# Performance work log

Measured on AMD Instinct MI355X. Metric: run time of the kernel, lower is better.

The kernel has to match this reference:

```python
import jax, jax.numpy as jnp
import numpy as np

DET_SIZE = 5120
DET_THRESHOLD = 0.5
NMS_THRESHOLD = 0.4
STRIDES = (8, 16, 32)
NUM_ANCHORS = 2
TOP_K = 2048  # fixed pre-NMS candidate count (jit-friendly stand-in for torch.where filtering)


def _anchor_centers(stride):
    n = DET_SIZE // stride
    g = jnp.arange(n, dtype=jnp.float32) * stride
    X, Y = jnp.meshgrid(g, g, indexing='xy')       # matches torch.meshgrid(..., indexing='xy')
    c = jnp.stack([X, Y], axis=-1).reshape(-1, 2)  # (n*n, 2), x fastest
    return jnp.repeat(c, NUM_ANCHORS, axis=0)      # stack([c]*2, dim=1).reshape(-1,2) == interleaved repeat


def _pairwise_iou(b):
    # b: (K,4) xyxy
    area = jnp.clip(b[:, 2] - b[:, 0], 0.0) * jnp.clip(b[:, 3] - b[:, 1], 0.0)
    lt = jnp.maximum(b[:, None, :2], b[None, :, :2])
    rb = jnp.minimum(b[:, None, 2:], b[None, :, 2:])
    wh = jnp.clip(rb - lt, 0.0)
    inter = wh[..., 0] * wh[..., 1]
    return inter / (area[:, None] + area[None, :] - inter + 1e-9)


def _forward(scores8, bbox8, lms8, scores16, bbox16, lms16, scores32, bbox32, lms32, det_scale):
    confs, boxes, lmss = [], [], []
    per_stride = [(scores8, bbox8, lms8), (scores16, bbox16, lms16), (scores32, bbox32, lms32)]
    for (conf, bbox, lms), stride in zip(per_stride, STRIDES):
        c = _anchor_centers(stride)                 # (N,2)
        b = bbox * stride                            # distance-style offsets scaled by stride
        l = lms * stride
        box = jnp.concatenate([c - b[:, :2], c + b[:, 2:4]], axis=-1) / det_scale  # (N,4) xyxy
        pts = (c[:, None, :] + l.reshape(-1, 5, 2)) / det_scale                    # (N,5,2)
        confs.append(conf.reshape(-1)); boxes.append(box); lmss.append(pts)
    conf = jnp.concatenate(confs)
    box = jnp.concatenate(boxes, axis=0)
    pts = jnp.concatenate(lmss, axis=0)
    # score threshold via masking (fixed shapes); below-threshold entries get conf=-1
    conf_m = jnp.where(conf >= DET_THRESHOLD, conf, -1.0)
    top_conf, top_idx = jax.lax.top_k(conf_m, TOP_K)
    top_box = box[top_idx]          # (K,4)
    top_pts = pts[top_idx]          # (K,5,2)
    valid = top_conf >= DET_THRESHOLD
    iou = _pairwise_iou(top_box)    # (K,K)
    later = jnp.arange(TOP_K)
    def body(i, keep):
        supp = (iou[i] > NMS_THRESHOLD) & (later > i) & keep[i] & valid[i]
        return keep & ~supp
    keep = jax.lax.fori_loop(0, TOP_K, body, valid)  # greedy NMS in descending-score order
    m = keep.astype(top_box.dtype)
    # (K, 15) = [conf | bbox(4) | lms(10)], suppressed/invalid rows zeroed
    return jnp.concatenate([(top_conf * m)[:, None], top_box * m[:, None], top_pts.reshape(TOP_K, 10) * m[:, None]], axis=-1)


def setup_inputs() -> dict:
    key = jax.random.key(0)
    ks = jax.random.split(key, 9)
    inp = {}
    for i, s in enumerate(STRIDES):
        n = DET_SIZE // s
        N = n * n * NUM_ANCHORS
        inp[f'scores{s}'] = jax.random.uniform(ks[3 * i], (N,), dtype=jnp.float32)
        inp[f'bbox{s}'] = jax.random.uniform(ks[3 * i + 1], (N, 4), dtype=jnp.float32) * 8.0
        inp[f'lms{s}'] = jax.random.normal(ks[3 * i + 2], (N, 10), dtype=jnp.float32) * 4.0
    inp['det_scale'] = jnp.array(0.5, dtype=jnp.float32)
    return inp


def reference(scores8, bbox8, lms8, scores16, bbox16, lms16, scores32, bbox32, lms32, det_scale):
    return _forward(scores8, bbox8, lms8, scores16, bbox16, lms16, scores32, bbox32, lms32, det_scale)
```

## Files before the change

kernel.cpp:

```cpp
#include <hip/hip_runtime.h>
#include <stdint.h>
#include <stddef.h>

#pragma clang fp contract(off)

#define N8   819200u
#define N16  204800u
#define N32  51200u
#define NTOT 1075200u
#define TOPK 2048
#define CAND_MAX 8192
#define NBIN 8192u
#define BINSHIFT 10
#define NMS_THR 0.4f
#define DET_THR 0.5f

#define OFF_HIST   0u
#define OFF_META   32768u
#define OFF_CAND   32832u
#define OFF_TIDX   98368u
#define OFF_TCONF  106560u
#define OFF_BOX    114752u
#define OFF_DIAG   147520u
#define OFF_SUPPT  155968u

__device__ __forceinline__ float load_conf(unsigned a, const float* __restrict__ s8,
                                           const float* __restrict__ s16,
                                           const float* __restrict__ s32) {
  if (a < N8) return s8[a];
  if (a < N8 + N16) return s16[a - N8];
  return s32[a - (N8 + N16)];
}

__device__ __forceinline__ void decode(unsigned a,
    const float* __restrict__ b8, const float* __restrict__ l8,
    const float* __restrict__ b16, const float* __restrict__ l16,
    const float* __restrict__ b32, const float* __restrict__ l32,
    float& cx, float& cy, float& s, const float*& bb, const float*& lm) {
  if (a < N8) {
    unsigned cell = a >> 1;
    cx = (float)((cell % 640u) * 8u); cy = (float)((cell / 640u) * 8u);
    s = 8.f; bb = b8 + (size_t)a * 4; lm = l8 + (size_t)a * 10;
  } else if (a < N8 + N16) {
    unsigned loc = a - N8; unsigned cell = loc >> 1;
    cx = (float)((cell % 320u) * 16u); cy = (float)((cell / 320u) * 16u);
    s = 16.f; bb = b16 + (size_t)loc * 4; lm = l16 + (size_t)loc * 10;
  } else {
    unsigned loc = a - (N8 + N16); unsigned cell = loc >> 1;
    cx = (float)((cell % 160u) * 32u); cy = (float)((cell / 160u) * 32u);
    s = 32.f; bb = b32 + (size_t)loc * 4; lm = l32 + (size_t)loc * 10;
  }
}

__global__ void k_hist(const float* __restrict__ s8, const float* __restrict__ s16,
                       const float* __restrict__ s32, unsigned* __restrict__ hist) {
  unsigned i = blockIdx.x * blockDim.x + threadIdx.x;
  unsigned st = gridDim.x * blockDim.x;
  for (unsigned a = i; a < NTOT; a += st) {
    float c = load_conf(a, s8, s16, s32);
    if (c >= DET_THR) {
      unsigned v = (__float_as_uint(c) - 0x3F000000u) >> BINSHIFT;
      if (v > NBIN - 1u) v = NBIN - 1u;
      atomicAdd(&hist[v], 1u);
    }
  }
}

__global__ void __launch_bounds__(1024) k_scan(const unsigned* __restrict__ hist,
                                               unsigned* __restrict__ meta) {
  __shared__ unsigned suf[1024];
  int t = threadIdx.x;
  const unsigned* hp = hist + (size_t)t * 8;
  unsigned s = 0;
  for (int b = 0; b < 8; b++) s += hp[b];
  suf[t] = s;
  __syncthreads();
  for (int d = 1; d < 1024; d <<= 1) {
    unsigned v = (t + d < 1024) ? suf[t + d] : 0u;
    __syncthreads();
    suf[t] += v;
    __syncthreads();
  }
  unsigned total = suf[0];
  unsigned mine = suf[t];
  unsigned nxt = (t < 1023) ? suf[t + 1] : 0u;
  if (total < (unsigned)TOPK) {
    if (t == 0) { meta[0] = 0u; meta[2] = total; }
    return;
  }
  if (mine >= (unsigned)TOPK && nxt < (unsigned)TOPK) {
    unsigned run = nxt, cut = (unsigned)t * 8u;
    for (int b = 7; b >= 0; b--) {
      run += hp[b];
      if (run >= (unsigned)TOPK) { cut = (unsigned)t * 8u + (unsigned)b; break; }
    }
    meta[0] = cut; meta[2] = total;
  }
}

__global__ void k_compact(const float* __restrict__ s8, const float* __restrict__ s16,
                          const float* __restrict__ s32, unsigned* __restrict__ meta,
                          unsigned long long* __restrict__ cand) {
  unsigned cut = meta[0];
  unsigned i = blockIdx.x * blockDim.x + threadIdx.x;
  unsigned st = gridDim.x * blockDim.x;
  for (unsigned a = i; a < NTOT; a += st) {
    float c = load_conf(a, s8, s16, s32);
    if (c >= DET_THR) {
      unsigned b = __float_as_uint(c);
      unsigned v = (b - 0x3F000000u) >> BINSHIFT;
      if (v >= cut) {
        unsigned pos = atomicAdd(&meta[3], 1u);
        if (pos < (unsigned)CAND_MAX)
          cand[pos] = ((unsigned long long)b << 32) |
                      (unsigned long long)(0xFFFFFFFFu - a);
      }
    }
  }
}

__global__ void __launch_bounds__(256) k_rank(
    const unsigned long long* __restrict__ cand, const unsigned* __restrict__ meta,
    const float* __restrict__ b8, const float* __restrict__ l8,
    const float* __restrict__ b16, const float* __restrict__ l16,
    const float* __restrict__ b32, const float* __restrict__ l32,
    const float* __restrict__ dsp,
    unsigned* __restrict__ tidx, float* __restrict__ tconf, float* __restrict__ box) {
  unsigned count = meta[3];
  if (count > (unsigned)CAND_MAX) count = (unsigned)CAND_MAX;
  unsigned wave = blockIdx.x * 4u + (threadIdx.x >> 6);
  unsigned lane = threadIdx.x & 63u;
  if (wave >= count) return;
  unsigned long long my = cand[wave];
  unsigned cnt = 0;
  for (unsigned i = lane; i < count; i += 64u)
    cnt += (cand[i] > my) ? 1u : 0u;
  for (int d = 32; d > 0; d >>= 1) cnt += __shfl_down(cnt, d);
  if (lane == 0 && cnt < (unsigned)TOPK) {
    unsigned r = cnt;
    unsigned a = 0xFFFFFFFFu - (unsigned)(my & 0xFFFFFFFFull);
    float conf = __uint_as_float((unsigned)(my >> 32));
    float cx, cy, s; const float* bb; const float* lm;
    decode(a, b8, l8, b16, l16, b32, l32, cx, cy, s, bb, lm);
    float ds = dsp[0];
    float b0 = bb[0] * s, b1 = bb[1] * s, b2 = bb[2] * s, b3 = bb[3] * s;
    box[r * 4 + 0] = (cx - b0) / ds;
    box[r * 4 + 1] = (cy - b1) / ds;
    box[r * 4 + 2] = (cx + b2) / ds;
    box[r * 4 + 3] = (cy + b3) / ds;
    tidx[r] = a; tconf[r] = conf;
  }
}

__global__ void __launch_bounds__(256) k_supp(const float* __restrict__ box,
                                              unsigned* __restrict__ supp_t,
                                              unsigned* __restrict__ diag32) {
  int i = blockIdx.x;
  const float4 bi = ((const float4*)box)[i];
  float ai = fmaxf(bi.z - bi.x, 0.f) * fmaxf(bi.w - bi.y, 0.f);
  int tid = threadIdx.x;
  int lane = tid & 63, wv = tid >> 6;
  int c = i >> 5, k = i & 31;
  for (int base = 0; base < TOPK; base += 256) {
    int j = base + tid;
    const float4 bj = ((const float4*)box)[j];
    float aj = fmaxf(bj.z - bj.x, 0.f) * fmaxf(bj.w - bj.y, 0.f);
    float ltx = fmaxf(bi.x, bj.x), lty = fmaxf(bi.y, bj.y);
    float rbx = fminf(bi.z, bj.z), rby = fminf(bi.w, bj.w);
    float w = fmaxf(rbx - ltx, 0.f), h = fmaxf(rby - lty, 0.f);
    float inter = w * h;
    float iou = inter / (ai + aj - inter + 1e-9f);
    bool pred = (iou > NMS_THR) && (j > i);
    unsigned long long word = __ballot(pred);
    int w64 = (base >> 6) + wv;
    if (lane == 0) {
      supp_t[c * 2048 + (2 * w64) * 32 + k]     = (unsigned)(word & 0xFFFFFFFFull);
      supp_t[c * 2048 + (2 * w64 + 1) * 32 + k] = (unsigned)(word >> 32);
      if (w64 == (i >> 6))
        diag32[i] = (unsigned)(word >> (((i >> 5) & 1) * 32));
    }
  }
}

__global__ void __launch_bounds__(256) k_nms_out(
    const unsigned* __restrict__ supp_t, const unsigned* __restrict__ diag32,
    const unsigned* __restrict__ meta,
    const unsigned* __restrict__ tidx, const float* __restrict__ tconf,
    const float* __restrict__ b8, const float* __restrict__ l8,
    const float* __restrict__ b16, const float* __restrict__ l16,
    const float* __restrict__ b32, const float* __restrict__ l32,
    const float* __restrict__ dsp, float* __restrict__ out) {
  __shared__ unsigned keepw[64];
  int tid = threadIdx.x;
  if (tid < 64) {
    int lane = tid;
    unsigned count = meta[3];
    if (count > (unsigned)TOPK) count = (unsigned)TOPK;
    unsigned lo = (unsigned)lane * 32u;
    unsigned kw = (count >= lo + 32u) ? 0xFFFFFFFFu
                : (count <= lo ? 0u : ((1u << (count - lo)) - 1u));
    const uint4* rp4 = (const uint4*)supp_t + (size_t)lane * 8;
    uint4 T0[8], T1[8], T2[8], T3[8];
    unsigned dga[32], dgb[32];

#define LOADT(BUF, C)                                                         \
  _Pragma("unroll") for (int q = 0; q < 8; q++)                               \
      BUF[q] = rp4[(size_t)((C) * 512 + q)];
#define LOADD(DBUF, C)                                                        \
  _Pragma("unroll") for (int k = 0; k < 32; k++)                              \
      DBUF[k] = diag32[(unsigned)((C) * 32 + k)];

    LOADT(T0, 0) LOADT(T1, 1) LOADT(T2, 2) LOADT(T3, 3)
    LOADD(dga, 0)

#define STEP(BUF, DCUR, DNXT, C)                                              \
  {                                                                           \
    unsigned w = __builtin_amdgcn_readlane(kw, (C));                          \
    _Pragma("unroll") for (int k = 0; k < 32; k++) {                          \
      unsigned d = __builtin_amdgcn_readfirstlane(DCUR[k]);                   \
      w &= ~(((w >> k) & 1u) ? d : 0u);                                       \
    }                                                                         \
    if ((C) + 1 < 64) { LOADD(DNXT, (C) + 1) }                                \
    unsigned acc = 0u;                                                        \
    _Pragma("unroll") for (int q = 0; q < 8; q++) {                           \
      unsigned m0 = (unsigned)((int)(w << (31 - (4 * q + 0))) >> 31);         \
      unsigned m1 = (unsigned)((int)(w << (31 - (4 * q + 1))) >> 31);         \
      unsigned m2 = (unsigned)((int)(w << (31 - (4 * q + 2))) >> 31);         \
      unsigned m3 = (unsigned)((int)(w << (31 - (4 * q + 3))) >> 31);         \
      acc |= BUF[q].x & m0;                                                   \
      acc |= BUF[q].y & m1;                                                   \
      acc |= BUF[q].z & m2;                                                   \
      acc |= BUF[q].w & m3;                                                   \
    }                                                                         \
    kw &= ~acc;                                                               \
    if ((C) + 4 < 64) { LOADT(BUF, (C) + 4) }                                 \
  }

#pragma unroll 1
    for (int c = 0; c < 64; c += 8) {
      STEP(T0, dga, dgb, c + 0)
      STEP(T1, dgb, dga, c + 1)
      STEP(T2, dga, dgb, c + 2)
      STEP(T3, dgb, dga, c + 3)
      STEP(T0, dga, dgb, c + 4)
      STEP(T1, dgb, dga, c + 5)
      STEP(T2, dga, dgb, c + 6)
      STEP(T3, dgb, dga, c + 7)
    }
#undef LOADT
#undef LOADD
#undef STEP
    keepw[lane] = kw;
  }
  __syncthreads();
  float ds = dsp[0];
  for (int r = tid; r < TOPK; r += 256) {
    bool kept = (keepw[r >> 5] >> (r & 31)) & 1u;
    float o[15];
    if (kept) {
      unsigned a = tidx[r];
      float cx, cy, s; const float* bb; const float* lm;
      decode(a, b8, l8, b16, l16, b32, l32, cx, cy, s, bb, lm);
      o[0] = tconf[r];
      float b0 = bb[0] * s, b1 = bb[1] * s, b2 = bb[2] * s, b3 = bb[3] * s;
      o[1] = (cx - b0) / ds;
      o[2] = (cy - b1) / ds;
      o[3] = (cx + b2) / ds;
      o[4] = (cy + b3) / ds;
      for (int p = 0; p < 5; p++) {
        float lx = lm[2 * p] * s, ly = lm[2 * p + 1] * s;
        o[5 + 2 * p] = (cx + lx) / ds;
        o[6 + 2 * p] = (cy + ly) / ds;
      }
    } else {
      for (int cc = 0; cc < 15; cc++) o[cc] = 0.f;
    }
    for (int cc = 0; cc < 15; cc++) out[(size_t)r * 15 + cc] = o[cc];
  }
}

extern "C" void kernel_launch(void* const* d_in, const int* in_sizes, int n_in,
                              void* d_out, int out_size, void* d_ws, size_t ws_size,
                              hipStream_t stream) {
  const float* s8  = (const float*)d_in[0];
  const float* b8  = (const float*)d_in[1];
  const float* l8  = (const float*)d_in[2];
  const float* s16 = (const float*)d_in[3];
  const float* b16 = (const float*)d_in[4];
  const float* l16 = (const float*)d_in[5];
  const float* s32 = (const float*)d_in[6];
  const float* b32 = (const float*)d_in[7];
  const float* l32 = (const float*)d_in[8];
  const float* dsp = (const float*)d_in[9];
  char* ws = (char*)d_ws;
  unsigned* hist = (unsigned*)(ws + OFF_HIST);
  unsigned* meta = (unsigned*)(ws + OFF_META);
  unsigned long long* cand = (unsigned long long*)(ws + OFF_CAND);
  unsigned* tidx = (unsigned*)(ws + OFF_TIDX);
  float* tconf = (float*)(ws + OFF_TCONF);
  float* box = (float*)(ws + OFF_BOX);
  unsigned* diag = (unsigned*)(ws + OFF_DIAG);
  unsigned* supp_t = (unsigned*)(ws + OFF_SUPPT);
  float* out = (float*)d_out;

  hipMemsetAsync(ws, 0, OFF_META + 64, stream);
  k_hist<<<2048, 256, 0, stream>>>(s8, s16, s32, hist);
  k_scan<<<1, 1024, 0, stream>>>(hist, meta);
  k_compact<<<2048, 256, 0, stream>>>(s8, s16, s32, meta, cand);
  k_rank<<<CAND_MAX / 4, 256, 0, stream>>>(cand, meta, b8, l8, b16, l16, b32, l32,
                                           dsp, tidx, tconf, box);
  k_supp<<<TOPK, 256, 0, stream>>>(box, supp_t, diag);
  k_nms_out<<<1, 256, 0, stream>>>(supp_t, diag, meta, tidx, tconf,
                                   b8, l8, b16, l16, b32, l32, dsp, out);
}
```

Baseline: 123.5 us.

## Transpose diagonal suppression words so NMS preloads them once into registers

The diagonal 32-bit suppression words are now stored transposed (chunk-major per lane), so each lane of the single NMS wave loads all 32 diagonal words for its own chunk once up front. The per-chunk step reads them with readlane instead of issuing 32 scalar-ish loads per chunk, which removes a global-load dependency from the serial critical path. The OR reduction is also split into four independent accumulators to shorten the dependency chain. It costs 32 extra VGPRs held for the whole loop.

```diff
diff --git a/kernel.cpp b/kernel.cpp
--- a/kernel.cpp
+++ b/kernel.cpp
@@ -21,7 +21,7 @@
 #define OFF_TIDX   98368u
 #define OFF_TCONF  106560u
 #define OFF_BOX    114752u
-#define OFF_DIAG   147520u
+#define OFF_DIAGT  147520u
 #define OFF_SUPPT  155968u
 
 __device__ __forceinline__ float load_conf(unsigned a, const float* __restrict__ s8,
@@ -154,7 +154,7 @@
 
 __global__ void __launch_bounds__(256) k_supp(const float* __restrict__ box,
                                               unsigned* __restrict__ supp_t,
-                                              unsigned* __restrict__ diag32) {
+                                              unsigned* __restrict__ diagT) {
   int i = blockIdx.x;
   const float4 bi = ((const float4*)box)[i];
   float ai = fmaxf(bi.z - bi.x, 0.f) * fmaxf(bi.w - bi.y, 0.f);
@@ -177,13 +177,13 @@
       supp_t[c * 2048 + (2 * w64) * 32 + k]     = (unsigned)(word & 0xFFFFFFFFull);
       supp_t[c * 2048 + (2 * w64 + 1) * 32 + k] = (unsigned)(word >> 32);
       if (w64 == (i >> 6))
-        diag32[i] = (unsigned)(word >> (((i >> 5) & 1) * 32));
+        diagT[k * 64 + c] = (unsigned)(word >> (((i >> 5) & 1) * 32));
     }
   }
 }
 
 __global__ void __launch_bounds__(256) k_nms_out(
-    const unsigned* __restrict__ supp_t, const unsigned* __restrict__ diag32,
+    const unsigned* __restrict__ supp_t, const unsigned* __restrict__ diagT,
     const unsigned* __restrict__ meta,
     const unsigned* __restrict__ tidx, const float* __restrict__ tconf,
     const float* __restrict__ b8, const float* __restrict__ l8,
@@ -201,54 +201,47 @@
                 : (count <= lo ? 0u : ((1u << (count - lo)) - 1u));
     const uint4* rp4 = (const uint4*)supp_t + (size_t)lane * 8;
     uint4 T0[8], T1[8], T2[8], T3[8];
-    unsigned dga[32], dgb[32];
+    unsigned dg[32];
 
 #define LOADT(BUF, C)                                                         \
   _Pragma("unroll") for (int q = 0; q < 8; q++)                               \
-      BUF[q] = rp4[(size_t)((C) * 512 + q)];
-#define LOADD(DBUF, C)                                                        \
-  _Pragma("unroll") for (int k = 0; k < 32; k++)                              \
-      DBUF[k] = diag32[(unsigned)((C) * 32 + k)];
-
+      BUF[q] = rp4[(size_t)(unsigned)((C) * 512 + q)];
+
+#pragma unroll
+    for (int k = 0; k < 32; k++) dg[k] = diagT[k * 64 + lane];
     LOADT(T0, 0) LOADT(T1, 1) LOADT(T2, 2) LOADT(T3, 3)
-    LOADD(dga, 0)
-
-#define STEP(BUF, DCUR, DNXT, C)                                              \
+
+#define STEP(BUF, CC)                                                         \
   {                                                                           \
-    unsigned w = __builtin_amdgcn_readlane(kw, (C));                          \
+    int cc = (CC);                                                            \
+    unsigned w = __builtin_amdgcn_readlane(kw, cc);                           \
     _Pragma("unroll") for (int k = 0; k < 32; k++) {                          \
-      unsigned d = __builtin_amdgcn_readfirstlane(DCUR[k]);                   \
+      unsigned d = __builtin_amdgcn_readlane(dg[k], cc);                      \
       w &= ~(((w >> k) & 1u) ? d : 0u);                                       \
     }                                                                         \
-    if ((C) + 1 < 64) { LOADD(DNXT, (C) + 1) }                                \
-    unsigned acc = 0u;                                                        \
+    unsigned acc0 = 0u, acc1 = 0u, acc2 = 0u, acc3 = 0u;                      \
     _Pragma("unroll") for (int q = 0; q < 8; q++) {                           \
       unsigned m0 = (unsigned)((int)(w << (31 - (4 * q + 0))) >> 31);         \
       unsigned m1 = (unsigned)((int)(w << (31 - (4 * q + 1))) >> 31);         \
       unsigned m2 = (unsigned)((int)(w << (31 - (4 * q + 2))) >> 31);         \
       unsigned m3 = (unsigned)((int)(w << (31 - (4 * q + 3))) >> 31);         \
-      acc |= BUF[q].x & m0;                                                   \
-      acc |= BUF[q].y & m1;                                                   \
-      acc |= BUF[q].z & m2;                                                   \
-      acc |= BUF[q].w & m3;                                                   \
+      acc0 |= BUF[q].x & m0;                                                  \
+      acc1 |= BUF[q].y & m1;                                                  \
+      acc2 |= BUF[q].z & m2;                                                  \
+      acc3 |= BUF[q].w & m3;                                                  \
     }                                                                         \
-    kw &= ~acc;                                                               \
-    if ((C) + 4 < 64) { LOADT(BUF, (C) + 4) }                                 \
+    kw &= ~((acc0 | acc1) | (acc2 | acc3));                                   \
+    if (cc + 4 < 64) { LOADT(BUF, cc + 4) }                                   \
   }
 
 #pragma unroll 1
-    for (int c = 0; c < 64; c += 8) {
-      STEP(T0, dga, dgb, c + 0)
-      STEP(T1, dgb, dga, c + 1)
-      STEP(T2, dga, dgb, c + 2)
-      STEP(T3, dgb, dga, c + 3)
-      STEP(T0, dga, dgb, c + 4)
-      STEP(T1, dgb, dga, c + 5)
-      STEP(T2, dga, dgb, c + 6)
-      STEP(T3, dgb, dga, c + 7)
+    for (int c = 0; c < 64; c += 4) {
+      STEP(T0, c + 0)
+      STEP(T1, c + 1)
+      STEP(T2, c + 2)
+      STEP(T3, c + 3)
     }
 #undef LOADT
-#undef LOADD
 #undef STEP
     keepw[lane] = kw;
   }
@@ -299,7 +292,7 @@
   unsigned* tidx = (unsigned*)(ws + OFF_TIDX);
   float* tconf = (float*)(ws + OFF_TCONF);
   float* box = (float*)(ws + OFF_BOX);
-  unsigned* diag = (unsigned*)(ws + OFF_DIAG);
+  unsigned* diagT = (unsigned*)(ws + OFF_DIAGT);
   unsigned* supp_t = (unsigned*)(ws + OFF_SUPPT);
   float* out = (float*)d_out;
 
@@ -309,7 +302,7 @@
   k_compact<<<2048, 256, 0, stream>>>(s8, s16, s32, meta, cand);
   k_rank<<<CAND_MAX / 4, 256, 0, stream>>>(cand, meta, b8, l8, b16, l16, b32, l32,
                                            dsp, tidx, tconf, box);
-  k_supp<<<TOPK, 256, 0, stream>>>(box, supp_t, diag);
-  k_nms_out<<<1, 256, 0, stream>>>(supp_t, diag, meta, tidx, tconf,
+  k_supp<<<TOPK, 256, 0, stream>>>(box, supp_t, diagT);
+  k_nms_out<<<1, 256, 0, stream>>>(supp_t, diagT, meta, tidx, tconf,
                                    b8, l8, b16, l16, b32, l32, dsp, out);
 }
```

Result: slower. 127.9 us (+3.5%).
